# Kernel optimization log

Hardware: AMD Instinct MI355X
Metric: run time of the kernel (lower is better)

Reference implementation:

```python
import jax, jax.numpy as jnp
import numpy as np

B, N, K = 4, 1500, 30
NODE_F, EDGE_F, H = 1024, 128, 128
L, NUM_RBF, NUM_POS, NHEADS = 4, 16, 16, 4
DH = H // NHEADS
LN_EPS = 1e-6


def setup_inputs() -> dict:
    key = jax.random.key(0)
    ks = jax.random.split(key, 16)
    g = lambda k, shp: jax.random.normal(k, shp, jnp.float32) / np.sqrt(shp[-2] if len(shp) > 1 else 1.0)
    return {
        'X': jax.random.normal(ks[0], (B, N, 3), jnp.float32) * 10.0,
        'V': jax.random.normal(ks[1], (B, N, NODE_F), jnp.float32),
        'mask': jnp.ones((B, N), jnp.float32),
        'W_v': g(ks[2], (NODE_F, H)), 'b_v': jnp.zeros((H,), jnp.float32),
        'W_e': g(ks[3], (EDGE_F, H)), 'b_e': jnp.zeros((H,), jnp.float32),
        'W_edge': g(ks[4], (NUM_POS + NUM_RBF, EDGE_F)),
        'ln_e_g': jnp.ones((EDGE_F,), jnp.float32), 'ln_e_b': jnp.zeros((EDGE_F,), jnp.float32),
        'Wq': g(ks[5], (L, H, H)), 'Wk': g(ks[6], (L, 2 * H, H)),
        'Wv_a': g(ks[7], (L, 2 * H, H)), 'Wo': g(ks[8], (L, H, H)),
        'ln1_g': jnp.ones((L, H), jnp.float32), 'ln1_b': jnp.zeros((L, H), jnp.float32),
        'ln2_g': jnp.ones((L, H), jnp.float32), 'ln2_b': jnp.zeros((L, H), jnp.float32),
        'W_ff1': g(ks[9], (L, H, 4 * H)), 'b_ff1': jnp.zeros((L, 4 * H), jnp.float32),
        'W_ff2': g(ks[10], (L, 4 * H, H)), 'b_ff2': jnp.zeros((L, H), jnp.float32),
        'W_out': g(ks[11], (H, 1)), 'b_out': jnp.zeros((1,), jnp.float32),
    }


def _layer_norm(x, gamma, beta):
    mu = jnp.mean(x, -1, keepdims=True)
    var = jnp.var(x, -1, keepdims=True)
    return gamma * (x - mu) / jnp.sqrt(var + LN_EPS) + beta


def _gather_nodes(nodes, idx):
    # nodes [B,N,C], idx [B,N,K] -> [B,N,K,C]
    return jax.vmap(lambda n, i: n[i])(nodes, idx)


def reference(X, V, mask, W_v, b_v, W_e, b_e, W_edge, ln_e_g, ln_e_b, Wq, Wk, Wv_a, Wo,
              ln1_g, ln1_b, ln2_g, ln2_b, W_ff1, b_ff1, W_ff2, b_ff2, W_out, b_out):
    # ---- EdgeFeatures: masked pairwise distances + kNN topk ----
    mask2 = mask[:, :, None] * mask[:, None, :]            # [B,N,N]
    dX = X[:, :, None, :] - X[:, None, :, :]               # [B,N,N,3]
    D = mask2 * jnp.sqrt(jnp.sum(dX * dX, -1) + 1e-6)
    D_adj = D + (1.0 - mask2) * jnp.max(D, -1, keepdims=True)
    negD, E_idx = jax.lax.top_k(-D_adj, K)                 # k smallest distances
    D_nb = -negD                                           # [B,N,K]
    # RBF of neighbor distances
    mu = jnp.linspace(0.0, 20.0, NUM_RBF)
    sigma = 20.0 / NUM_RBF
    rbf = jnp.exp(-(((D_nb[..., None] - mu) / sigma) ** 2))  # [B,N,K,NUM_RBF]
    # sinusoidal relative positional encodings of neighbor offsets
    ii = jnp.arange(N, dtype=jnp.float32)[None, :, None]
    d_rel = (E_idx.astype(jnp.float32) - ii)[..., None]
    freq = jnp.exp(jnp.arange(0, NUM_POS, 2, dtype=jnp.float32) * (-np.log(10000.0) / NUM_POS))
    ang = d_rel * freq
    pos = jnp.concatenate([jnp.cos(ang), jnp.sin(ang)], -1)  # [B,N,K,NUM_POS]
    E = jnp.concatenate([pos, rbf], -1) @ W_edge
    E = _layer_norm(E, ln_e_g, ln_e_b)                     # [B,N,K,EDGE_F]
    # ---- node / edge embeddings ----
    h_V = V @ W_v + b_v                                    # [B,N,H]
    h_E = E @ W_e + b_e                                    # [B,N,K,H]
    mask_attend = mask[:, :, None] * _gather_nodes(mask[..., None], E_idx)[..., 0]  # [B,N,K]
    neg_inf = jnp.float32(np.finfo(np.float32).min)
    # ---- encoder layers ----
    for l in range(L):
        h_EV = jnp.concatenate([h_E, _gather_nodes(h_V, E_idx)], -1)  # [B,N,K,2H]
        Q = (h_V @ Wq[l]).reshape(B, N, NHEADS, DH)
        Kh = (h_EV @ Wk[l]).reshape(B, N, K, NHEADS, DH)
        Vh = (h_EV @ Wv_a[l]).reshape(B, N, K, NHEADS, DH)
        logits = jnp.einsum('bnhd,bnkhd->bnhk', Q, Kh) / np.sqrt(DH)
        m = mask_attend[:, :, None, :]                     # [B,N,1,K]
        attend = jax.nn.softmax(jnp.where(m > 0, logits, neg_inf), -1) * m
        upd = jnp.einsum('bnhk,bnkhd->bnhd', attend, Vh).reshape(B, N, H) @ Wo[l]
        h_V = _layer_norm(h_V + upd, ln1_g[l], ln1_b[l])
        dh = jax.nn.relu(h_V @ W_ff1[l] + b_ff1[l]) @ W_ff2[l] + b_ff2[l]
        h_V = _layer_norm(h_V + dh, ln2_g[l], ln2_b[l])
        h_V = mask[..., None] * h_V
    return (h_V @ W_out + b_out)[..., 0]                   # [B,N] logits
```

## Files before the change

kernel.cpp:

```cpp
#include <hip/hip_runtime.h>
#include <hip/hip_bf16.h>
#include <math.h>

#define NB 4
#define NN 1500
#define KNB 30
#define H 128
#define NHEADS 4
#define FFH 512
#define NODE_FEAT 1024
#define NROWS (NB*NN)
#define LN_EPS 1e-6f

#define P_F32_STRIDE 384
#define P_BF16_STRIDE 768

typedef __attribute__((ext_vector_type(8))) short s8v;
typedef __attribute__((ext_vector_type(4))) float f4v;

__device__ __forceinline__ float bf_lo(unsigned u){ union{unsigned i; float f;} v; v.i = u<<16; return v.f; }
__device__ __forceinline__ float bf_hi(unsigned u){ union{unsigned i; float f;} v; v.i = u & 0xffff0000u; return v.f; }

__device__ __forceinline__ void find_bucket30(
    const unsigned* hist, int base0, int t, int lane, int wave,
    int* wsum, int* res)
{
    int h[16], s = 0;
    const uint4* hp = (const uint4*)&hist[(t & 127) * 16];
    int sh = (t >> 7) << 4;
    uint4 w[4] = {hp[0], hp[1], hp[2], hp[3]};
#pragma unroll
    for (int i = 0; i < 4; i++) {
        h[i*4+0] = (w[i].x >> sh) & 0xffff;
        h[i*4+1] = (w[i].y >> sh) & 0xffff;
        h[i*4+2] = (w[i].z >> sh) & 0xffff;
        h[i*4+3] = (w[i].w >> sh) & 0xffff;
        s += h[i*4+0] + h[i*4+1] + h[i*4+2] + h[i*4+3];
    }
    int inc = s;
#pragma unroll
    for (int off = 1; off < 64; off <<= 1) {
        int o = __shfl_up(inc, off, 64);
        if (lane >= off) inc += o;
    }
    if (lane == 63) wsum[wave] = inc;
    __syncthreads();
    int base = base0 + inc - s;
    for (int w2 = 0; w2 < wave; w2++) base += wsum[w2];
    if (base < KNB && base + s >= KNB) {
        int running = base;
#pragma unroll
        for (int i = 0; i < 16; i++) {
            if (running < KNB && running + h[i] >= KNB) { res[0] = (t<<4)|i; res[1] = running; break; }
            running += h[i];
        }
    }
    __syncthreads();
}

__global__ __launch_bounds__(256) void topk_kernel(
    const float* __restrict__ X, const float* __restrict__ mask,
    int* __restrict__ E_idx, float* __restrict__ D_nb)
{
    int row = blockIdx.x;
    int b = row / NN;
    int t = threadIdx.x;
    int wave = t >> 6, lane = t & 63;
    __shared__ float d_adj[NN];
    __shared__ unsigned hist[2048];
    __shared__ float redw[4];
    __shared__ int   wsum[4];
    __shared__ int   res[2];
    __shared__ int   cand[64];
    __shared__ int   ncand;

    float xi0 = X[row*3+0], xi1 = X[row*3+1], xi2 = X[row*3+2];
    float mi = mask[row];

    float dr[6], m2r[6];
    float lmax = -1e30f;
#pragma unroll
    for (int q = 0; q < 6; q++) {
        int j = t + q*256;
        float d = 0.f, m2 = 0.f;
        if (j < NN) {
            float dx = xi0 - X[(b*NN+j)*3+0];
            float dy = xi1 - X[(b*NN+j)*3+1];
            float dz = xi2 - X[(b*NN+j)*3+2];
            d  = sqrtf(dx*dx + dy*dy + dz*dz + 1e-6f);
            m2 = mi * mask[b*NN+j];
            lmax = fmaxf(lmax, m2*d);
        }
        dr[q] = d; m2r[q] = m2;
    }
    for (int q = t; q < 2048; q += 256) hist[q] = 0;
#pragma unroll
    for (int off = 32; off > 0; off >>= 1)
        lmax = fmaxf(lmax, __shfl_xor(lmax, off, 64));
    if (lane == 0) redw[wave] = lmax;
    if (t == 0) ncand = 0;
    __syncthreads();
    float rowmax = fmaxf(fmaxf(redw[0], redw[1]), fmaxf(redw[2], redw[3]));

    unsigned kreg[6];
#pragma unroll
    for (int q = 0; q < 6; q++) {
        int j = t + q*256;
        if (j < NN) {
            float dv = m2r[q]*dr[q] + (1.0f - m2r[q])*rowmax;
            d_adj[j] = dv;
            unsigned key = __float_as_uint(dv);
            kreg[q] = key;
            unsigned bkt = key >> 20;
            atomicAdd(&hist[bkt & 2047], 1u << ((bkt >> 11) << 4));
        } else kreg[q] = 0xFFFFFFFFu;
    }
    __syncthreads();

    find_bucket30(hist, 0, t, lane, wave, wsum, res);
    int B1 = res[0], nb1 = res[1];

    for (int q = t; q < 2048; q += 256) hist[q] = 0;
    __syncthreads();
#pragma unroll
    for (int q = 0; q < 6; q++) {
        if ((kreg[q] >> 20) == (unsigned)B1) {
            unsigned bkt = (kreg[q] >> 8) & 0xFFF;
            atomicAdd(&hist[bkt & 2047], 1u << ((bkt >> 11) << 4));
        }
    }
    __syncthreads();

    find_bucket30(hist, nb1, t, lane, wave, wsum, res);
    unsigned Bfull = ((unsigned)B1 << 12) | (unsigned)res[0];

#pragma unroll
    for (int q = 0; q < 6; q++) {
        if ((kreg[q] >> 8) <= Bfull) {
            int slot = atomicAdd(&ncand, 1);
            if (slot < 64) cand[slot] = t + q*256;
        }
    }
    __syncthreads();

    if (wave == 0) {
        int nc = min(ncand, 64);
        if (lane < nc) {
            int j = cand[lane];
            float v = d_adj[j];
            int rank = 0;
            for (int m = 0; m < nc; m++) {
                int jm = cand[m];
                float vm = d_adj[jm];
                rank += (vm < v || (vm == v && jm < j)) ? 1 : 0;
            }
            if (rank < KNB) {
                E_idx[row*KNB + rank] = j;
                D_nb[row*KNB + rank]  = v;
            }
        }
    }
}

__global__ __launch_bounds__(256) void wprep_edge_kernel(
    const float* __restrict__ W_edge, __hip_bfloat16* __restrict__ W_edge_t)
{
    int tid = blockIdx.x*256 + threadIdx.x;
    int n = tid >> 5, k = tid & 31;
    W_edge_t[tid] = __float2bfloat16(W_edge[k*H + n]);
}

__global__ __launch_bounds__(256) void edge_kernel(
    const int* __restrict__ E_idx, const float* __restrict__ D_nb,
    const __hip_bfloat16* __restrict__ W_edge_t, const float* __restrict__ ln_g,
    const float* __restrict__ ln_b, __hip_bfloat16* __restrict__ E_ln)
{
    int g0 = blockIdx.x * 2;
    int t = threadIdx.x;
    int wave = t >> 6, lane = t & 63, lm = lane & 15, lq = lane >> 4;
    __shared__ __hip_bfloat16 Es[64*136];

    int row = wave*16 + lm;
    int rr = row < 60 ? row : 59;
    int node = g0 + (rr >= KNB ? 1 : 0);
    int e = node*KNB + (rr >= KNB ? rr - KNB : rr);
    float drel = (float)(E_idx[e] - (node % NN));
    float dnb  = D_nb[e];

    const float FR[8] = {1.f, 0.31622776601683794f, 0.1f, 0.031622776601683794f,
                         0.01f, 0.0031622776601683794f, 0.001f, 0.00031622776601683794f};
    union { s8v v; __hip_bfloat16 h[8]; } af;
    if (lq == 0) {
#pragma unroll
        for (int j = 0; j < 8; j++) af.h[j] = __float2bfloat16(cosf(drel*FR[j]));
    } else if (lq == 1) {
#pragma unroll
        for (int j = 0; j < 8; j++) af.h[j] = __float2bfloat16(sinf(drel*FR[j]));
    } else {
        int f0 = (lq-2)*8;
#pragma unroll
        for (int j = 0; j < 8; j++) {
            float mu = (20.0f/15.0f) * (float)(f0+j);
            float z = (dnb - mu) * 0.8f;
            af.h[j] = __float2bfloat16(expf(-z*z));
        }
    }

    f4v acc[8];
#pragma unroll
    for (int nt = 0; nt < 8; nt++) {
        s8v bf = *(const s8v*)&W_edge_t[(nt*16+lm)*32 + lq*8];
        f4v z = {0.f,0.f,0.f,0.f};
        acc[nt] = __builtin_amdgcn_mfma_f32_16x16x32_bf16(af.v, bf, z, 0,0,0);
    }

    float gv[8], bv[8];
#pragma unroll
    for (int nt = 0; nt < 8; nt++) { gv[nt] = ln_g[nt*16+lm]; bv[nt] = ln_b[nt*16+lm]; }
#pragma unroll
    for (int r = 0; r < 4; r++) {
        float sm = 0.f, sq = 0.f;
#pragma unroll
        for (int nt = 0; nt < 8; nt++) { float x = acc[nt][r]; sm += x; sq += x*x; }
#pragma unroll
        for (int m = 1; m < 16; m <<= 1) {
            sm += __shfl_xor(sm, m, 64);
            sq += __shfl_xor(sq, m, 64);
        }
        float mu = sm * (1.0f/H);
        float rs = rsqrtf(sq*(1.0f/H) - mu*mu + LN_EPS);
        int erow = wave*16 + lq*4 + r;
#pragma unroll
        for (int nt = 0; nt < 8; nt++)
            Es[erow*136 + nt*16 + lm] =
                __float2bfloat16(gv[nt]*(acc[nt][r]-mu)*rs + bv[nt]);
    }
    __syncthreads();

    __hip_bfloat16* dst = E_ln + (size_t)g0*KNB*H;
    for (int q = t; q < 960; q += 256) {
        int r = q >> 4, c8 = (q & 15) * 8;
        *(s8v*)&dst[r*H + c8] = *(const s8v*)&Es[r*136 + c8];
    }
}

__global__ __launch_bounds__(256) void wprep_v_kernel(
    const float* __restrict__ W_v, __hip_bfloat16* __restrict__ Wv_t)
{
    int tid = blockIdx.x*256 + threadIdx.x;
    int n = tid & 127, k = tid >> 7;
    Wv_t[(size_t)n*NODE_FEAT + k] = __float2bfloat16(W_v[k*H + n]);
}

__global__ __launch_bounds__(128) void wprep_kv_kernel(
    const float* __restrict__ W_e, const float* __restrict__ b_e,
    const float* __restrict__ Wk, const float* __restrict__ Wv,
    float* __restrict__ Wkv_f, float* __restrict__ bias_kv)
{
    int l = blockIdx.x >> 8;
    int n = blockIdx.x & 255;
    int t = threadIdx.x;
    int col = n & 127;
    const float* W = (n < 128) ? (Wk + l*2*H*H) : (Wv + l*2*H*H);
    __shared__ float wcol[128];
    wcol[t] = W[t*H + col];
    __syncthreads();
    float a = 0.f;
    for (int c = 0; c < H; c += 4) {
        float4 we = *(const float4*)&W_e[t*H + c];
        a += we.x*wcol[c] + we.y*wcol[c+1] + we.z*wcol[c+2] + we.w*wcol[c+3];
    }
    Wkv_f[(size_t)(l*256 + n)*H + t] = a;
    if (t == 0) {
        float bsum = 0.f;
        for (int c = 0; c < H; c++) bsum += b_e[c]*wcol[c];
        bias_kv[l*256 + n] = bsum;
    }
}

__global__ __launch_bounds__(128) void wprep_qp_kernel(
    const float* __restrict__ Wq, const float* __restrict__ Wkv_f,
    __hip_bfloat16* __restrict__ Wn_t)
{
    int l = blockIdx.x >> 9;
    int m = blockIdx.x & 511;
    int h = m >> 7, e = m & 127;
    int c = threadIdx.x;
    __shared__ float wek[32];
    if (c < 32) wek[c] = Wkv_f[(size_t)(l*256 + h*32 + c)*H + e];
    __syncthreads();
    const float* wq = Wq + (size_t)l*16384 + c*128 + h*32;
    float a = 0.f;
#pragma unroll
    for (int d = 0; d < 32; d++) a += wq[d]*wek[d];
    Wn_t[(size_t)(l*896 + 128 + m)*H + c] = __float2bfloat16(a);
}

__global__ __launch_bounds__(128) void wprep_op_kernel(
    const float* __restrict__ Wo, const float* __restrict__ Wkv_f,
    __hip_bfloat16* __restrict__ WoU_t)
{
    int l = blockIdx.x / 640;
    int kk = blockIdx.x - l*640;
    int n = threadIdx.x;
    __shared__ float wev[32];
    if (kk < 512) {
        int h = kk >> 7;
        int e = kk & 127;
        if (n < 32) wev[n] = Wkv_f[(size_t)(l*256 + 128 + h*32 + n)*H + e];
    }
    __syncthreads();
    float v;
    if (kk < 512) {
        int h = kk >> 7;
        float a = 0.f;
#pragma unroll
        for (int d = 0; d < 32; d++)
            a += wev[d]*Wo[(size_t)l*16384 + (h*32+d)*128 + n];
        v = a;
    } else {
        v = Wo[(size_t)l*16384 + (kk-512)*128 + n];
    }
    WoU_t[((size_t)l*128 + n)*640 + kk] = __float2bfloat16(v);
}

__global__ __launch_bounds__(256) void wprep_post_kernel(
    const float* __restrict__ Wf1, const float* __restrict__ Wf2,
    const float* __restrict__ Wq, const float* __restrict__ Wk,
    const float* __restrict__ Wv,
    __hip_bfloat16* __restrict__ Wf1_t, __hip_bfloat16* __restrict__ Wf2_t,
    __hip_bfloat16* __restrict__ Wn_t)
{
    int id = blockIdx.x*256 + threadIdx.x;
    int l = id / 180224;
    int r = id - l*180224;
    float v; __hip_bfloat16* dst;
    if (r < 65536) {
        int n = r >> 7, k = r & 127;
        v = Wf1[(size_t)l*65536 + k*512 + n];
        dst = Wf1_t + (size_t)l*65536 + r;
    } else if (r < 131072) {
        int rr = r - 65536;
        int n = rr >> 9, k = rr & 511;
        v = Wf2[(size_t)l*65536 + k*128 + n];
        dst = Wf2_t + (size_t)l*65536 + rr;
    } else if (r < 147456) {
        int rr = r - 131072;
        int n = rr >> 7, k = rr & 127;
        v = Wq[(size_t)l*16384 + k*128 + n];
        dst = Wn_t + (size_t)l*114688 + rr;
    } else {
        int rr = r - 147456;
        int n = rr >> 7, k = rr & 127;
        v = (n < 128) ? Wk[(size_t)l*32768 + (128+k)*128 + n]
                      : Wv[(size_t)l*32768 + (128+k)*128 + (n-128)];
        dst = Wn_t + (size_t)l*114688 + 81920 + rr;
    }
    *dst = __float2bfloat16(v);
}

__global__ __launch_bounds__(512) void hv_init_kernel(
    const float* __restrict__ V, const __hip_bfloat16* __restrict__ Wv_t,
    const float* __restrict__ b_v, float* __restrict__ hv,
    const __hip_bfloat16* __restrict__ Wn_t, float* __restrict__ P,
    __hip_bfloat16* __restrict__ PKV)
{
    int row0 = blockIdx.x * 32;
    int t = threadIdx.x;
    int wave = t >> 6, lane = t & 63, lm = lane & 15, lq = lane >> 4;
    __shared__ __hip_bfloat16 Vs[32*1032];
    __shared__ __hip_bfloat16 zs[32*136];

    for (int q = t; q < 8192; q += 512) {
        int r = q >> 8, c4 = (q & 255) * 4;
        int gr = row0 + r; if (gr > NROWS-1) gr = NROWS-1;
        float4 v4 = *(const float4*)&V[(size_t)gr*NODE_FEAT + c4];
        union { ushort u[4]; uint2 w; } pk;
        pk.u[0] = __bfloat16_as_ushort(__float2bfloat16(v4.x));
        pk.u[1] = __bfloat16_as_ushort(__float2bfloat16(v4.y));
        pk.u[2] = __bfloat16_as_ushort(__float2bfloat16(v4.z));
        pk.u[3] = __bfloat16_as_ushort(__float2bfloat16(v4.w));
        *(uint2*)&Vs[r*1032 + c4] = pk.w;
    }
    __syncthreads();

    {
        int cc = wave*16 + lm;
        float b = b_v[cc];
        f4v a0 = {0.f,0.f,0.f,0.f}, a1 = a0;
        for (int ks = 0; ks < 32; ks++) {
            s8v wf = *(const s8v*)&Wv_t[(size_t)(wave*16+lm)*NODE_FEAT + ks*32 + lq*8];
            s8v f0 = *(const s8v*)&Vs[lm*1032 + ks*32 + lq*8];
            s8v f1 = *(const s8v*)&Vs[(16+lm)*1032 + ks*32 + lq*8];
            a0 = __builtin_amdgcn_mfma_f32_16x16x32_bf16(f0, wf, a0, 0,0,0);
            a1 = __builtin_amdgcn_mfma_f32_16x16x32_bf16(f1, wf, a1, 0,0,0);
        }
#pragma unroll
        for (int r = 0; r < 4; r++) {
            int rr0 = lq*4 + r, rr1 = 16 + lq*4 + r;
            int g0 = row0 + rr0, g1 = row0 + rr1;
            float v0 = a0[r] + b, v1 = a1[r] + b;
            if (g0 < NROWS) hv[(size_t)g0*H + cc] = v0;
            if (g1 < NROWS) hv[(size_t)g1*H + cc] = v1;
            zs[rr0*136+cc] = __float2bfloat16(v0);
            zs[rr1*136+cc] = __float2bfloat16(v1);
        }
    }
    __syncthreads();

    __hip_bfloat16* Pb = (__hip_bfloat16*)P;
    for (int ntl = 0; ntl < 7; ntl++) {
        int nt = wave*7 + ntl;
        int cc = nt*16 + lm;
        f4v a0 = {0.f,0.f,0.f,0.f}, a1 = a0;
#pragma unroll
        for (int ks = 0; ks < 4; ks++) {
            s8v wf = *(const s8v*)&Wn_t[(size_t)(nt*16+lm)*H + ks*32 + lq*8];
            s8v f0 = *(const s8v*)&zs[lm*136 + ks*32 + lq*8];
            s8v f1 = *(const s8v*)&zs[(16+lm)*136 + ks*32 + lq*8];
            a0 = __builtin_amdgcn_mfma_f32_16x16x32_bf16(f0, wf, a0, 0,0,0);
            a1 = __builtin_amdgcn_mfma_f32_16x16x32_bf16(f1, wf, a1, 0,0,0);
        }
#pragma unroll
        for (int mt = 0; mt < 2; mt++) {
            f4v* ap = mt ? &a1 : &a0;
#pragma unroll
            for (int r = 0; r < 4; r++) {
                int rr = row0 + mt*16 + lq*4 + r;
                if (rr < NROWS) {
                    float av = (*ap)[r];
                    if (cc < 128)
                        P[(size_t)rr*P_F32_STRIDE + cc] = av;
                    else if (cc < 640)
                        Pb[(size_t)rr*P_BF16_STRIDE + 128 + cc] = __float2bfloat16(av);
                    else
                        PKV[(size_t)rr*256 + (cc-640)] = __float2bfloat16(av);
                }
            }
        }
    }
}

__global__ __launch_bounds__(256) void attn_kernel(
    const __hip_bfloat16* __restrict__ E_ln, const float* __restrict__ biasv,
    float* __restrict__ P, const __hip_bfloat16* __restrict__ PKV,
    const int* __restrict__ E_idx, const float* __restrict__ mask)
{
    int g0 = blockIdx.x * 2;
    int t = threadIdx.x;
    int wave = t >> 6, lane = t & 63, lm = lane & 15, lq = lane >> 4;
    __shared__ __hip_bfloat16 Es[60*136];
    __shared__ float Qs[2*128];
    __shared__ __hip_bfloat16 Qp[2*512];
    __shared__ float att_s[2*128];
    __shared__ float ssum[8];
    __shared__ float mv_s[60];
    __shared__ int   nbr[60];

    const __hip_bfloat16* hebase = E_ln + (size_t)g0*KNB*H;
    for (int q = t; q < 960; q += 256) {
        int r = q >> 4, c8 = (q & 15) * 8;
        *(s8v*)&Es[r*136 + c8] = *(const s8v*)&hebase[r*H + c8];
    }
    const __hip_bfloat16* Pb = (const __hip_bfloat16*)P;
    if (t < 128) {
        int node = t >> 6, c8 = (t & 63)*8;
        *(s8v*)&Qp[node*512 + c8] = *(const s8v*)&Pb[(size_t)(g0+node)*P_BF16_STRIDE + 256 + c8];
    }
    {
        int node = t >> 7, c = t & 127;
        Qs[t] = P[(size_t)(g0+node)*P_F32_STRIDE + c];
    }
    if (t < 60) {
        int gn = g0 + t/30;
        int b = gn / NN;
        int idx = E_idx[gn*KNB + (t%30)];
        nbr[t]  = b*NN + idx;
        mv_s[t] = mask[gn] * mask[b*NN + idx];
    }
    __syncthreads();

    if (t < 240) {
        int node = t/120, tt = t%120, h = tt/30, kk = tt%30;
        const uint4* ep = (const uint4*)&Es[(node*30+kk)*136];
        const uint4* qp = (const uint4*)&Qp[node*512 + h*128];
        float a = 0.f;
#pragma unroll
        for (int j = 0; j < 16; j++) {
            uint4 e4 = ep[j], q4 = qp[j];
            a += bf_lo(e4.x)*bf_lo(q4.x) + bf_hi(e4.x)*bf_hi(q4.x);
            a += bf_lo(e4.y)*bf_lo(q4.y) + bf_hi(e4.y)*bf_hi(q4.y);
            a += bf_lo(e4.z)*bf_lo(q4.z) + bf_hi(e4.z)*bf_hi(q4.z);
            a += bf_lo(e4.w)*bf_lo(q4.w) + bf_hi(e4.w)*bf_hi(q4.w);
        }
        const uint4* kb = (const uint4*)(PKV + (size_t)nbr[node*30+kk]*256 + h*32);
        const float* q = &Qs[node*128 + h*32];
#pragma unroll
        for (int j = 0; j < 4; j++) {
            uint4 u = kb[j];
            const float* q8 = q + j*8;
            a += q8[0]*bf_lo(u.x) + q8[1]*bf_hi(u.x)
               + q8[2]*bf_lo(u.y) + q8[3]*bf_hi(u.y)
               + q8[4]*bf_lo(u.z) + q8[5]*bf_hi(u.z)
               + q8[6]*bf_lo(u.w) + q8[7]*bf_hi(u.w);
        }
        int r = node*30 + kk;
        att_s[node*128 + h*32 + kk] =
            (mv_s[r] > 0.f) ? a*0.17677669529663687f : -3.4028235e38f;
    }
    __syncthreads();

    if (wave < 2) {
        int node = wave, h = lq, j = lm;
        float* ap = &att_s[node*128 + h*32];
        const float* mp = &mv_s[node*30];
        float a0 = ap[j];
        float a1 = (j+16 < KNB) ? ap[j+16] : -3.4028235e38f;
        float mx = fmaxf(a0, a1);
#pragma unroll
        for (int m = 1; m < 16; m <<= 1) mx = fmaxf(mx, __shfl_xor(mx, m, 64));
        float e0 = __expf(a0 - mx);
        float e1 = (j+16 < KNB) ? __expf(a1 - mx) : 0.f;
        float s = e0 + e1;
#pragma unroll
        for (int m = 1; m < 16; m <<= 1) s += __shfl_xor(s, m, 64);
        float inv = 1.0f / s;
        float w0 = e0 * inv * mp[j];
        float w1 = (j+16 < KNB) ? e1 * inv * mp[j+16] : 0.f;
        ap[j] = w0;
        if (j+16 < KNB) ap[j+16] = w1;
        float ss = w0 + w1;
#pragma unroll
        for (int m = 1; m < 16; m <<= 1) ss += __shfl_xor(ss, m, 64);
        if (j == 0) ssum[node*4 + h] = ss;
    }
    __syncthreads();

    {
        int node = t >> 7, c = t & 127, h = c >> 5;
        __hip_bfloat16* Ub = (__hip_bfloat16*)P + (size_t)(g0+node)*P_BF16_STRIDE;
        const float* ap = &att_s[node*128];
        const int* nb = &nbr[node*30];

        float u = ssum[node*4 + h] * biasv[c];
        const float* ah = ap + h*32;
        for (int k = 0; k < KNB; k++)
            u += ah[k] * __bfloat162float(PKV[(size_t)nb[k]*256 + 128 + c]);
        Ub[512 + c] = __float2bfloat16(u);

        float s0 = 0.f, s1 = 0.f, s2 = 0.f, s3 = 0.f;
        for (int k = 0; k < KNB; k++) {
            float e = __bfloat162float(Es[(node*30+k)*136 + c]);
            s0 += ap[k]      * e;
            s1 += ap[32+k]   * e;
            s2 += ap[64+k]   * e;
            s3 += ap[96+k]   * e;
        }
        Ub[c]       = __float2bfloat16(s0);
        Ub[128 + c] = __float2bfloat16(s1);
        Ub[256 + c] = __float2bfloat16(s2);
        Ub[384 + c] = __float2bfloat16(s3);
    }
}

__global__ __launch_bounds__(512) void post_kernel(
    float* __restrict__ hv, float* __restrict__ P,
    __hip_bfloat16* __restrict__ PKV, const float* __restrict__ mask,
    const __hip_bfloat16* __restrict__ WoU_t,
    const float* __restrict__ ln1g, const float* __restrict__ ln1b,
    const float* __restrict__ ln2g, const float* __restrict__ ln2b,
    const __hip_bfloat16* __restrict__ Wf1_t, const float* __restrict__ bf1,
    const __hip_bfloat16* __restrict__ Wf2_t, const float* __restrict__ bf2,
    const __hip_bfloat16* __restrict__ Wn_t,
    const float* __restrict__ W_out, const float* __restrict__ b_out,
    float* __restrict__ out)
{
    int row0 = blockIdx.x * 32;
    int t = threadIdx.x;
    int wave = t >> 6, lane = t & 63, lm = lane & 15, lq = lane >> 4;

    __shared__ __hip_bfloat16 AusT1[32*648];
    __shared__ float xs[32*132];
    __shared__ __hip_bfloat16 yz[32*136];
    __hip_bfloat16* Aus = AusT1;
    __hip_bfloat16* t1  = AusT1;

    const __hip_bfloat16* Pbc = (const __hip_bfloat16*)P;
    for (int q = t; q < 2560; q += 512) {
        int r = q/80, c8 = (q%80)*8;
        int gr = row0 + r; if (gr > NROWS-1) gr = NROWS-1;
        *(s8v*)&Aus[r*648 + c8] = *(const s8v*)&Pbc[(size_t)gr*P_BF16_STRIDE + c8];
    }
    __syncthreads();

    {
        int cc = wave*16 + lm;
        f4v a0 = {0.f,0.f,0.f,0.f}, a1 = a0;
        for (int ks = 0; ks < 20; ks++) {
            s8v wf = *(const s8v*)&WoU_t[(size_t)(wave*16+lm)*640 + ks*32 + lq*8];
            s8v f0 = *(const s8v*)&Aus[lm*648 + ks*32 + lq*8];
            s8v f1 = *(const s8v*)&Aus[(16+lm)*648 + ks*32 + lq*8];
            a0 = __builtin_amdgcn_mfma_f32_16x16x32_bf16(f0, wf, a0, 0,0,0);
            a1 = __builtin_amdgcn_mfma_f32_16x16x32_bf16(f1, wf, a1, 0,0,0);
        }
#pragma unroll
        for (int r = 0; r < 4; r++) {
            int rr0 = lq*4 + r, rr1 = 16 + lq*4 + r;
            int g0 = row0 + rr0; if (g0 > NROWS-1) g0 = NROWS-1;
            int g1 = row0 + rr1; if (g1 > NROWS-1) g1 = NROWS-1;
            xs[rr0*132+cc] = hv[(size_t)g0*128 + cc] + a0[r];
            xs[rr1*132+cc] = hv[(size_t)g1*128 + cc] + a1[r];
        }
    }
    __syncthreads();

    {
        float g0 = ln1g[lane], g1 = ln1g[64+lane];
        float b0 = ln1b[lane], b1 = ln1b[64+lane];
#pragma unroll
        for (int i = 0; i < 4; i++) {
            int r = wave*4 + i;
            float x0 = xs[r*132 + lane], x1 = xs[r*132 + 64 + lane];
            float sm = x0 + x1, sq = x0*x0 + x1*x1;
#pragma unroll
            for (int m = 1; m < 64; m <<= 1) {
                sm += __shfl_xor(sm, m, 64);
                sq += __shfl_xor(sq, m, 64);
            }
            float mu = sm*(1.0f/H);
            float rs = rsqrtf(sq*(1.0f/H) - mu*mu + LN_EPS);
            float v0 = g0*(x0-mu)*rs + b0, v1 = g1*(x1-mu)*rs + b1;
            xs[r*132 + lane] = v0; xs[r*132 + 64 + lane] = v1;
            yz[r*136 + lane] = __float2bfloat16(v0);
            yz[r*136 + 64 + lane] = __float2bfloat16(v1);
        }
    }
    __syncthreads();

    for (int ntl = 0; ntl < 4; ntl++) {
        int nt = wave*4 + ntl;
        int cc = nt*16 + lm;
        float b = bf1[cc];
        f4v a0 = {0.f,0.f,0.f,0.f}, a1 = a0;
#pragma unroll
        for (int ks = 0; ks < 4; ks++) {
            s8v wf = *(const s8v*)&Wf1_t[(size_t)(nt*16+lm)*128 + ks*32 + lq*8];
            s8v f0 = *(const s8v*)&yz[lm*136 + ks*32 + lq*8];
            s8v f1 = *(const s8v*)&yz[(16+lm)*136 + ks*32 + lq*8];
            a0 = __builtin_amdgcn_mfma_f32_16x16x32_bf16(f0, wf, a0, 0,0,0);
            a1 = __builtin_amdgcn_mfma_f32_16x16x32_bf16(f1, wf, a1, 0,0,0);
        }
#pragma unroll
        for (int r = 0; r < 4; r++) {
            t1[(lq*4+r)*520 + cc]      = __float2bfloat16(fmaxf(a0[r]+b, 0.f));
            t1[(16+lq*4+r)*520 + cc]   = __float2bfloat16(fmaxf(a1[r]+b, 0.f));
        }
    }
    __syncthreads();

    {
        int cc = wave*16 + lm;
        float b = bf2[cc];
        f4v a0 = {0.f,0.f,0.f,0.f}, a1 = a0;
        for (int ks = 0; ks < 16; ks++) {
            s8v wf = *(const s8v*)&Wf2_t[(size_t)(wave*16+lm)*512 + ks*32 + lq*8];
            s8v f0 = *(const s8v*)&t1[lm*520 + ks*32 + lq*8];
            s8v f1 = *(const s8v*)&t1[(16+lm)*520 + ks*32 + lq*8];
            a0 = __builtin_amdgcn_mfma_f32_16x16x32_bf16(f0, wf, a0, 0,0,0);
            a1 = __builtin_amdgcn_mfma_f32_16x16x32_bf16(f1, wf, a1, 0,0,0);
        }
#pragma unroll
        for (int r = 0; r < 4; r++) {
            int rr0 = lq*4 + r, rr1 = 16 + lq*4 + r;
            xs[rr0*132+cc] = xs[rr0*132+cc] + a0[r] + b;
            xs[rr1*132+cc] = xs[rr1*132+cc] + a1[r] + b;
        }
    }
    __syncthreads();

    {
        float g0 = ln2g[lane], g1 = ln2g[64+lane];
        float b0 = ln2b[lane], b1 = ln2b[64+lane];
        float wo0 = 0.f, wo1 = 0.f, bo = 0.f;
        if (!Wn_t) { wo0 = W_out[lane]; wo1 = W_out[64+lane]; bo = b_out[0]; }
#pragma unroll
        for (int i = 0; i < 4; i++) {
            int r = wave*4 + i;
            int gr = row0 + r;
            float mk = mask[gr > NROWS-1 ? NROWS-1 : gr];
            float x0 = xs[r*132 + lane], x1 = xs[r*132 + 64 + lane];
            float sm = x0 + x1, sq = x0*x0 + x1*x1;
#pragma unroll
            for (int m = 1; m < 64; m <<= 1) {
                sm += __shfl_xor(sm, m, 64);
                sq += __shfl_xor(sq, m, 64);
            }
            float mu = sm*(1.0f/H);
            float rs = rsqrtf(sq*(1.0f/H) - mu*mu + LN_EPS);
            float v0 = mk*(g0*(x0-mu)*rs + b0), v1 = mk*(g1*(x1-mu)*rs + b1);
            yz[r*136 + lane] = __float2bfloat16(v0);
            yz[r*136 + 64 + lane] = __float2bfloat16(v1);
            if (gr < NROWS) {
                hv[(size_t)gr*128 + lane] = v0;
                hv[(size_t)gr*128 + 64 + lane] = v1;
            }
            if (!Wn_t) {
                float o = v0*wo0 + v1*wo1;
#pragma unroll
                for (int m = 1; m < 64; m <<= 1) o += __shfl_xor(o, m, 64);
                if (lane == 0 && gr < NROWS) out[gr] = o + bo;
            }
        }
    }
    __syncthreads();

    if (Wn_t) {
        __hip_bfloat16* Pbw = (__hip_bfloat16*)P;
        for (int ntl = 0; ntl < 7; ntl++) {
            int nt = wave*7 + ntl;
            int cc = nt*16 + lm;
            f4v a0 = {0.f,0.f,0.f,0.f}, a1 = a0;
#pragma unroll
            for (int ks = 0; ks < 4; ks++) {
                s8v wf = *(const s8v*)&Wn_t[(size_t)(nt*16+lm)*128 + ks*32 + lq*8];
                s8v f0 = *(const s8v*)&yz[lm*136 + ks*32 + lq*8];
                s8v f1 = *(const s8v*)&yz[(16+lm)*136 + ks*32 + lq*8];
                a0 = __builtin_amdgcn_mfma_f32_16x16x32_bf16(f0, wf, a0, 0,0,0);
                a1 = __builtin_amdgcn_mfma_f32_16x16x32_bf16(f1, wf, a1, 0,0,0);
            }
#pragma unroll
            for (int mt = 0; mt < 2; mt++) {
                f4v* ap = mt ? &a1 : &a0;
#pragma unroll
                for (int r = 0; r < 4; r++) {
                    int rr = row0 + mt*16 + lq*4 + r;
                    if (rr < NROWS) {
                        float av = (*ap)[r];
                        if (cc < 128)
                            P[(size_t)rr*P_F32_STRIDE + cc] = av;
                        else if (cc < 640)
                            Pbw[(size_t)rr*P_BF16_STRIDE + 128 + cc] = __float2bfloat16(av);
                        else
                            PKV[(size_t)rr*256 + (cc-640)] = __float2bfloat16(av);
                    }
                }
            }
        }
    }
}

extern "C" void kernel_launch(void* const* d_in, const int* in_sizes, int n_in,
                              void* d_out, int out_size, void* d_ws, size_t ws_size,
                              hipStream_t stream)
{
    const float* X      = (const float*)d_in[0];
    const float* V      = (const float*)d_in[1];
    const float* mask   = (const float*)d_in[2];
    const float* W_v    = (const float*)d_in[3];
    const float* b_v    = (const float*)d_in[4];
    const float* W_e    = (const float*)d_in[5];
    const float* b_e    = (const float*)d_in[6];
    const float* W_edge = (const float*)d_in[7];
    const float* ln_e_g = (const float*)d_in[8];
    const float* ln_e_b = (const float*)d_in[9];
    const float* Wq     = (const float*)d_in[10];
    const float* Wk     = (const float*)d_in[11];
    const float* Wv_a   = (const float*)d_in[12];
    const float* Wo     = (const float*)d_in[13];
    const float* ln1g   = (const float*)d_in[14];
    const float* ln1b   = (const float*)d_in[15];
    const float* ln2g   = (const float*)d_in[16];
    const float* ln2b   = (const float*)d_in[17];
    const float* Wf1    = (const float*)d_in[18];
    const float* bf1    = (const float*)d_in[19];
    const float* Wf2    = (const float*)d_in[20];
    const float* bf2    = (const float*)d_in[21];
    const float* W_out  = (const float*)d_in[22];
    const float* b_out  = (const float*)d_in[23];
    float* out = (float*)d_out;

    char* ws = (char*)d_ws;
    int*            E_idx    = (int*)ws;
    float*          D_nb     = (float*)(ws + 720000);
    __hip_bfloat16* E_ln     = (__hip_bfloat16*)(ws + 1440000);
    float*          hv       = (float*)(ws + 47520000);
    float*          bias_kv  = (float*)(ws + 50592000);
    float*          Wkv_f    = (float*)(ws + 50596096);
    __hip_bfloat16* Wn_t     = (__hip_bfloat16*)(ws + 51120384);
    __hip_bfloat16* WoU_t    = (__hip_bfloat16*)(ws + 52037888);
    __hip_bfloat16* Wf1_t    = (__hip_bfloat16*)(ws + 52693248);
    __hip_bfloat16* Wf2_t    = (__hip_bfloat16*)(ws + 53217536);
    __hip_bfloat16* Wv_t     = (__hip_bfloat16*)(ws + 53741824);
    __hip_bfloat16* W_edge_t = (__hip_bfloat16*)(ws + 54003968);
    __hip_bfloat16* PKV      = (__hip_bfloat16*)(ws + 54012160);
    float*          P        = (float*)(ws + 57084160);

    topk_kernel<<<NROWS, 256, 0, stream>>>(X, mask, E_idx, D_nb);
    wprep_edge_kernel<<<16, 256, 0, stream>>>(W_edge, W_edge_t);
    edge_kernel<<<NROWS/2, 256, 0, stream>>>(E_idx, D_nb, W_edge_t, ln_e_g, ln_e_b, E_ln);
    wprep_kv_kernel<<<1024, 128, 0, stream>>>(W_e, b_e, Wk, Wv_a, Wkv_f, bias_kv);
    wprep_qp_kernel<<<2048, 128, 0, stream>>>(Wq, Wkv_f, Wn_t);
    wprep_op_kernel<<<2560, 128, 0, stream>>>(Wo, Wkv_f, WoU_t);
    wprep_post_kernel<<<2816, 256, 0, stream>>>(Wf1, Wf2, Wq, Wk, Wv_a,
                                                Wf1_t, Wf2_t, Wn_t);
    wprep_v_kernel<<<512, 256, 0, stream>>>(W_v, Wv_t);
    hv_init_kernel<<<(NROWS+31)/32, 512, 0, stream>>>(V, Wv_t, b_v, hv, Wn_t, P, PKV);

    for (int l = 0; l < 4; l++) {
        attn_kernel<<<NROWS/2, 256, 0, stream>>>(
            E_ln, bias_kv + l*256 + 128, P, PKV, E_idx, mask);
        post_kernel<<<(NROWS+31)/32, 512, 0, stream>>>(
            hv, P, PKV, mask, WoU_t + (size_t)l*81920,
            ln1g + l*H, ln1b + l*H, ln2g + l*H, ln2b + l*H,
            Wf1_t + (size_t)l*65536, bf1 + l*FFH,
            Wf2_t + (size_t)l*65536, bf2 + l*H,
            (l < 3) ? (Wn_t + (size_t)(l+1)*114688) : (const __hip_bfloat16*)nullptr,
            W_out, b_out, out);
    }
}
```

Baseline: 419.8 us.

## Fold edge projection and LayerNorm into query to shrink attention logit dot product

The edge-key part of the attention logit is rewritten algebraically. The LayerNorm'd edge feature dotted with the projected query becomes rs*(raw32-dim features · Q·M) - mu*rs*(Q·gamma-sum), with M = (Wk_e·gamma)·W_edge precomputed per layer. Attention now recomputes the 32 positional/RBF features per edge and does a 32-wide dot instead of a 128-wide one over E_ln. This cuts the per-node query projection outputs from 512 to 128+4 columns, and edge_kernel additionally stores per-edge LN statistics. In exchange, attn recomputes sin/cos/exp per edge and adds precision differences from folding bf16 weights.

```diff
diff --git a/kernel.cpp b/kernel.cpp
--- a/kernel.cpp
+++ b/kernel.cpp
@@ -14,6 +14,8 @@
 
 #define P_F32_STRIDE 384
 #define P_BF16_STRIDE 768
+
+#define WNT_STRIDE 67584
 
 typedef __attribute__((ext_vector_type(8))) short s8v;
 typedef __attribute__((ext_vector_type(4))) float f4v;
@@ -173,7 +175,8 @@
 __global__ __launch_bounds__(256) void edge_kernel(
     const int* __restrict__ E_idx, const float* __restrict__ D_nb,
     const __hip_bfloat16* __restrict__ W_edge_t, const float* __restrict__ ln_g,
-    const float* __restrict__ ln_b, __hip_bfloat16* __restrict__ E_ln)
+    const float* __restrict__ ln_b, __hip_bfloat16* __restrict__ E_ln,
+    float* __restrict__ EMS)
 {
     int g0 = blockIdx.x * 2;
     int t = threadIdx.x;
@@ -230,6 +233,10 @@
         float mu = sm * (1.0f/H);
         float rs = rsqrtf(sq*(1.0f/H) - mu*mu + LN_EPS);
         int erow = wave*16 + lq*4 + r;
+        if (lm == 0 && erow < 60) {
+            EMS[(g0*KNB + erow)*2]     = rs;
+            EMS[(g0*KNB + erow)*2 + 1] = mu*rs;
+        }
 #pragma unroll
         for (int nt = 0; nt < 8; nt++)
             Es[erow*136 + nt*16 + lm] =
@@ -278,22 +285,51 @@
     }
 }
 
-__global__ __launch_bounds__(128) void wprep_qp_kernel(
-    const float* __restrict__ Wq, const float* __restrict__ Wkv_f,
-    __hip_bfloat16* __restrict__ Wn_t)
-{
-    int l = blockIdx.x >> 9;
-    int m = blockIdx.x & 511;
-    int h = m >> 7, e = m & 127;
-    int c = threadIdx.x;
-    __shared__ float wek[32];
-    if (c < 32) wek[c] = Wkv_f[(size_t)(l*256 + h*32 + c)*H + e];
-    __syncthreads();
-    const float* wq = Wq + (size_t)l*16384 + c*128 + h*32;
+__global__ __launch_bounds__(128) void wprep_m_kernel(
+    const float* __restrict__ Wkv_f, const float* __restrict__ W_edge,
+    const float* __restrict__ ln_e_g,
+    float* __restrict__ M_buf, float* __restrict__ vg_buf)
+{
+    int l = blockIdx.x >> 7;
+    int n = blockIdx.x & 127;
+    int t = threadIdx.x;
+    __shared__ float wg_s[128];
+    wg_s[t] = Wkv_f[(size_t)(l*256 + n)*H + t] * ln_e_g[t];
+    __syncthreads();
+    if (t < 32) {
+        float a = 0.f;
+        for (int e = 0; e < 128; e++) a += wg_s[e] * W_edge[t*H + e];
+        M_buf[((size_t)(l*128 + n))*32 + t] = a;
+    } else if (t == 32) {
+        float a = 0.f;
+        for (int e = 0; e < 128; e++) a += wg_s[e];
+        vg_buf[l*128 + n] = a;
+    }
+}
+
+__global__ __launch_bounds__(128) void wprep_q2_kernel(
+    const float* __restrict__ Wq, const float* __restrict__ M_buf,
+    const float* __restrict__ vg_buf, __hip_bfloat16* __restrict__ Wn_t)
+{
+    int l = blockIdx.x >> 7;
+    int c = blockIdx.x & 127;
+    int t = threadIdx.x;
+    int h = t >> 5, f = t & 31;
+    __shared__ float wq_s[128];
+    wq_s[t] = Wq[(size_t)l*16384 + c*128 + t];
+    __syncthreads();
     float a = 0.f;
 #pragma unroll
-    for (int d = 0; d < 32; d++) a += wq[d]*wek[d];
-    Wn_t[(size_t)(l*896 + 128 + m)*H + c] = __float2bfloat16(a);
+    for (int d = 0; d < 32; d++)
+        a += wq_s[h*32 + d] * M_buf[((size_t)(l*128 + h*32 + d))*32 + f];
+    Wn_t[(size_t)l*WNT_STRIDE + (128 + t)*H + c] = __float2bfloat16(a);
+    if (t < 4) {
+        float b = 0.f;
+        for (int d = 0; d < 32; d++)
+            b += wq_s[t*32 + d] * vg_buf[l*128 + t*32 + d];
+        Wn_t[(size_t)l*WNT_STRIDE + (256 + t)*H + c] = __float2bfloat16(b);
+    }
+    if (t < 12) Wn_t[(size_t)l*WNT_STRIDE + (260 + t)*H + c] = __float2bfloat16(0.f);
 }
 
 __global__ __launch_bounds__(128) void wprep_op_kernel(
@@ -348,13 +384,13 @@
         int rr = r - 131072;
         int n = rr >> 7, k = rr & 127;
         v = Wq[(size_t)l*16384 + k*128 + n];
-        dst = Wn_t + (size_t)l*114688 + rr;
+        dst = Wn_t + (size_t)l*WNT_STRIDE + rr;
     } else {
         int rr = r - 147456;
         int n = rr >> 7, k = rr & 127;
         v = (n < 128) ? Wk[(size_t)l*32768 + (128+k)*128 + n]
                       : Wv[(size_t)l*32768 + (128+k)*128 + (n-128)];
-        dst = Wn_t + (size_t)l*114688 + 81920 + rr;
+        dst = Wn_t + (size_t)l*WNT_STRIDE + 272*H + rr;
     }
     *dst = __float2bfloat16(v);
 }
@@ -363,7 +399,7 @@
     const float* __restrict__ V, const __hip_bfloat16* __restrict__ Wv_t,
     const float* __restrict__ b_v, float* __restrict__ hv,
     const __hip_bfloat16* __restrict__ Wn_t, float* __restrict__ P,
-    __hip_bfloat16* __restrict__ PKV)
+    __hip_bfloat16* __restrict__ PKV, float* __restrict__ qg_buf)
 {
     int row0 = blockIdx.x * 32;
     int t = threadIdx.x;
@@ -409,8 +445,9 @@
     __syncthreads();
 
     __hip_bfloat16* Pb = (__hip_bfloat16*)P;
-    for (int ntl = 0; ntl < 7; ntl++) {
-        int nt = wave*7 + ntl;
+    for (int ntl = 0; ntl < 5; ntl++) {
+        int nt = wave*5 + ntl;
+        if (nt >= 33) break;
         int cc = nt*16 + lm;
         f4v a0 = {0.f,0.f,0.f,0.f}, a1 = a0;
 #pragma unroll
@@ -431,10 +468,12 @@
                     float av = (*ap)[r];
                     if (cc < 128)
                         P[(size_t)rr*P_F32_STRIDE + cc] = av;
-                    else if (cc < 640)
-                        Pb[(size_t)rr*P_BF16_STRIDE + 128 + cc] = __float2bfloat16(av);
-                    else
-                        PKV[(size_t)rr*256 + (cc-640)] = __float2bfloat16(av);
+                    else if (cc < 256)
+                        Pb[(size_t)rr*P_BF16_STRIDE + 640 + (cc-128)] = __float2bfloat16(av);
+                    else if (cc < 272) {
+                        if (cc < 260) qg_buf[rr*4 + (cc-256)] = av;
+                    } else
+                        PKV[(size_t)rr*256 + (cc-272)] = __float2bfloat16(av);
                 }
             }
         }
@@ -444,17 +483,22 @@
 __global__ __launch_bounds__(256) void attn_kernel(
     const __hip_bfloat16* __restrict__ E_ln, const float* __restrict__ biasv,
     float* __restrict__ P, const __hip_bfloat16* __restrict__ PKV,
-    const int* __restrict__ E_idx, const float* __restrict__ mask)
+    const int* __restrict__ E_idx, const float* __restrict__ D_nb,
+    const float* __restrict__ EMS, const float* __restrict__ qg_buf,
+    const float* __restrict__ mask)
 {
     int g0 = blockIdx.x * 2;
     int t = threadIdx.x;
     int wave = t >> 6, lane = t & 63, lm = lane & 15, lq = lane >> 4;
     __shared__ __hip_bfloat16 Es[60*136];
+    __shared__ __hip_bfloat16 Ps[60*40];
+    __shared__ __hip_bfloat16 Qps[2*136];
     __shared__ float Qs[2*128];
-    __shared__ __hip_bfloat16 Qp[2*512];
     __shared__ float att_s[2*128];
     __shared__ float ssum[8];
     __shared__ float mv_s[60];
+    __shared__ float rs_s[60], murs_s[60];
+    __shared__ float qgs[8];
     __shared__ int   nbr[60];
 
     const __hip_bfloat16* hebase = E_ln + (size_t)g0*KNB*H;
@@ -463,9 +507,9 @@
         *(s8v*)&Es[r*136 + c8] = *(const s8v*)&hebase[r*H + c8];
     }
     const __hip_bfloat16* Pb = (const __hip_bfloat16*)P;
-    if (t < 128) {
-        int node = t >> 6, c8 = (t & 63)*8;
-        *(s8v*)&Qp[node*512 + c8] = *(const s8v*)&Pb[(size_t)(g0+node)*P_BF16_STRIDE + 256 + c8];
+    if (t < 32) {
+        int node = t >> 4, c8 = (t & 15)*8;
+        *(s8v*)&Qps[node*136 + c8] = *(const s8v*)&Pb[(size_t)(g0+node)*P_BF16_STRIDE + 640 + c8];
     }
     {
         int node = t >> 7, c = t & 127;
@@ -477,23 +521,54 @@
         int idx = E_idx[gn*KNB + (t%30)];
         nbr[t]  = b*NN + idx;
         mv_s[t] = mask[gn] * mask[b*NN + idx];
+        float2 em = ((const float2*)EMS)[g0*KNB + t];
+        rs_s[t] = em.x; murs_s[t] = em.y;
+    }
+    if (t < 8) qgs[t] = qg_buf[(g0 + (t>>2))*4 + (t&3)];
+    if (t < 240) {
+        int r = t >> 2, seg = t & 3;
+        int gn = g0 + r/30;
+        int e = gn*KNB + (r%30);
+        float drel = (float)(E_idx[e] - (gn % NN));
+        float dnb  = D_nb[e];
+        const float FR[8] = {1.f, 0.31622776601683794f, 0.1f, 0.031622776601683794f,
+                             0.01f, 0.0031622776601683794f, 0.001f, 0.00031622776601683794f};
+        union { s8v v; __hip_bfloat16 h[8]; } pf;
+        if (seg == 0) {
+#pragma unroll
+            for (int j = 0; j < 8; j++) pf.h[j] = __float2bfloat16(cosf(drel*FR[j]));
+        } else if (seg == 1) {
+#pragma unroll
+            for (int j = 0; j < 8; j++) pf.h[j] = __float2bfloat16(sinf(drel*FR[j]));
+        } else {
+            int f0 = (seg-2)*8;
+#pragma unroll
+            for (int j = 0; j < 8; j++) {
+                float mu = (20.0f/15.0f) * (float)(f0+j);
+                float z = (dnb - mu) * 0.8f;
+                pf.h[j] = __float2bfloat16(expf(-z*z));
+            }
+        }
+        *(s8v*)&Ps[r*40 + seg*8] = pf.v;
     }
     __syncthreads();
 
     if (t < 240) {
         int node = t/120, tt = t%120, h = tt/30, kk = tt%30;
-        const uint4* ep = (const uint4*)&Es[(node*30+kk)*136];
-        const uint4* qp = (const uint4*)&Qp[node*512 + h*128];
+        int r = node*30 + kk;
+        const uint4* pp = (const uint4*)&Ps[r*40];
+        const uint4* qp = (const uint4*)&Qps[node*136 + h*32];
         float a = 0.f;
 #pragma unroll
-        for (int j = 0; j < 16; j++) {
-            uint4 e4 = ep[j], q4 = qp[j];
+        for (int j = 0; j < 4; j++) {
+            uint4 e4 = pp[j], q4 = qp[j];
             a += bf_lo(e4.x)*bf_lo(q4.x) + bf_hi(e4.x)*bf_hi(q4.x);
             a += bf_lo(e4.y)*bf_lo(q4.y) + bf_hi(e4.y)*bf_hi(q4.y);
             a += bf_lo(e4.z)*bf_lo(q4.z) + bf_hi(e4.z)*bf_hi(q4.z);
             a += bf_lo(e4.w)*bf_lo(q4.w) + bf_hi(e4.w)*bf_hi(q4.w);
         }
-        const uint4* kb = (const uint4*)(PKV + (size_t)nbr[node*30+kk]*256 + h*32);
+        a = rs_s[r]*a - murs_s[r]*qgs[node*4 + h];
+        const uint4* kb = (const uint4*)(PKV + (size_t)nbr[r]*256 + h*32);
         const float* q = &Qs[node*128 + h*32];
 #pragma unroll
         for (int j = 0; j < 4; j++) {
@@ -504,7 +579,6 @@
                + q8[4]*bf_lo(u.z) + q8[5]*bf_hi(u.z)
                + q8[6]*bf_lo(u.w) + q8[7]*bf_hi(u.w);
         }
-        int r = node*30 + kk;
         att_s[node*128 + h*32 + kk] =
             (mv_s[r] > 0.f) ? a*0.17677669529663687f : -3.4028235e38f;
     }
@@ -565,7 +639,8 @@
 
 __global__ __launch_bounds__(512) void post_kernel(
     float* __restrict__ hv, float* __restrict__ P,
-    __hip_bfloat16* __restrict__ PKV, const float* __restrict__ mask,
+    __hip_bfloat16* __restrict__ PKV, float* __restrict__ qg_buf,
+    const float* __restrict__ mask,
     const __hip_bfloat16* __restrict__ WoU_t,
     const float* __restrict__ ln1g, const float* __restrict__ ln1b,
     const float* __restrict__ ln2g, const float* __restrict__ ln2b,
@@ -716,8 +791,9 @@
 
     if (Wn_t) {
         __hip_bfloat16* Pbw = (__hip_bfloat16*)P;
-        for (int ntl = 0; ntl < 7; ntl++) {
-            int nt = wave*7 + ntl;
+        for (int ntl = 0; ntl < 5; ntl++) {
+            int nt = wave*5 + ntl;
+            if (nt >= 33) break;
             int cc = nt*16 + lm;
             f4v a0 = {0.f,0.f,0.f,0.f}, a1 = a0;
 #pragma unroll
@@ -738,10 +814,12 @@
                         float av = (*ap)[r];
                         if (cc < 128)
                             P[(size_t)rr*P_F32_STRIDE + cc] = av;
-                        else if (cc < 640)
-                            Pbw[(size_t)rr*P_BF16_STRIDE + 128 + cc] = __float2bfloat16(av);
-                        else
-                            PKV[(size_t)rr*256 + (cc-640)] = __float2bfloat16(av);
+                        else if (cc < 256)
+                            Pbw[(size_t)rr*P_BF16_STRIDE + 640 + (cc-128)] = __float2bfloat16(av);
+                        else if (cc < 272) {
+                            if (cc < 260) qg_buf[rr*4 + (cc-256)] = av;
+                        } else
+                            PKV[(size_t)rr*256 + (cc-272)] = __float2bfloat16(av);
                     }
                 }
             }
@@ -794,27 +872,32 @@
     __hip_bfloat16* W_edge_t = (__hip_bfloat16*)(ws + 54003968);
     __hip_bfloat16* PKV      = (__hip_bfloat16*)(ws + 54012160);
     float*          P        = (float*)(ws + 57084160);
+    float*          EMS      = (float*)(ws + 66300160);
+    float*          M_buf    = (float*)(ws + 67740160);
+    float*          vg_buf   = (float*)(ws + 67805696);
+    float*          qg_buf   = (float*)(ws + 67807744);
 
     topk_kernel<<<NROWS, 256, 0, stream>>>(X, mask, E_idx, D_nb);
     wprep_edge_kernel<<<16, 256, 0, stream>>>(W_edge, W_edge_t);
-    edge_kernel<<<NROWS/2, 256, 0, stream>>>(E_idx, D_nb, W_edge_t, ln_e_g, ln_e_b, E_ln);
+    edge_kernel<<<NROWS/2, 256, 0, stream>>>(E_idx, D_nb, W_edge_t, ln_e_g, ln_e_b, E_ln, EMS);
     wprep_kv_kernel<<<1024, 128, 0, stream>>>(W_e, b_e, Wk, Wv_a, Wkv_f, bias_kv);
-    wprep_qp_kernel<<<2048, 128, 0, stream>>>(Wq, Wkv_f, Wn_t);
+    wprep_m_kernel<<<512, 128, 0, stream>>>(Wkv_f, W_edge, ln_e_g, M_buf, vg_buf);
+    wprep_q2_kernel<<<512, 128, 0, stream>>>(Wq, M_buf, vg_buf, Wn_t);
     wprep_op_kernel<<<2560, 128, 0, stream>>>(Wo, Wkv_f, WoU_t);
     wprep_post_kernel<<<2816, 256, 0, stream>>>(Wf1, Wf2, Wq, Wk, Wv_a,
                                                 Wf1_t, Wf2_t, Wn_t);
     wprep_v_kernel<<<512, 256, 0, stream>>>(W_v, Wv_t);
-    hv_init_kernel<<<(NROWS+31)/32, 512, 0, stream>>>(V, Wv_t, b_v, hv, Wn_t, P, PKV);
+    hv_init_kernel<<<(NROWS+31)/32, 512, 0, stream>>>(V, Wv_t, b_v, hv, Wn_t, P, PKV, qg_buf);
 
     for (int l = 0; l < 4; l++) {
         attn_kernel<<<NROWS/2, 256, 0, stream>>>(
-            E_ln, bias_kv + l*256 + 128, P, PKV, E_idx, mask);
+            E_ln, bias_kv + l*256 + 128, P, PKV, E_idx, D_nb, EMS, qg_buf, mask);
         post_kernel<<<(NROWS+31)/32, 512, 0, stream>>>(
-            hv, P, PKV, mask, WoU_t + (size_t)l*81920,
+            hv, P, PKV, qg_buf, mask, WoU_t + (size_t)l*81920,
             ln1g + l*H, ln1b + l*H, ln2g + l*H, ln2b + l*H,
             Wf1_t + (size_t)l*65536, bf1 + l*FFH,
             Wf2_t + (size_t)l*65536, bf2 + l*H,
-            (l < 3) ? (Wn_t + (size_t)(l+1)*114688) : (const __hip_bfloat16*)nullptr,
+            (l < 3) ? (Wn_t + (size_t)(l+1)*WNT_STRIDE) : (const __hip_bfloat16*)nullptr,
             W_out, b_out, out);
     }
 }
```

New measurement: 450.7 us. 1.07x slower.
